# Kernel optimization log

Hardware: AMD Instinct MI355X
Metric: run time of the kernel (lower is better)

The kernel has to match this reference:

```python
import jax, jax.numpy as jnp
import numpy as np

B_CHUNK = 5          # hardcoded self.B in the module
GAMMA = 0.9865
BATCH, SEQ, FEAT, DIM = 8, 4000, 256, 256


def setup_inputs() -> dict:
    key = jax.random.key(0)
    ks = jax.random.split(key, 6)
    xq = jax.random.normal(ks[0], (BATCH, SEQ, FEAT), jnp.float32)
    xk = jax.random.normal(ks[1], (BATCH, SEQ, FEAT), jnp.float32)
    xv = jax.random.normal(ks[2], (BATCH, SEQ, FEAT), jnp.float32)
    scale = 1.0 / np.sqrt(FEAT).astype(np.float32)
    Wq = jax.random.normal(ks[3], (FEAT, DIM), jnp.float32) * scale
    Wk = jax.random.normal(ks[4], (FEAT, DIM), jnp.float32) * scale
    Wv = jax.random.normal(ks[5], (FEAT, DIM), jnp.float32) * scale
    return {"xq": xq, "xk": xk, "xv": xv, "Wq": Wq, "Wk": Wk, "Wv": Wv}


def reference(xq, xk, xv, Wq, Wk, Wv):
    gamma = jnp.float32(GAMMA)
    B = B_CHUNK
    b, seq, _ = xq.shape
    dim = Wq.shape[1]
    n = seq // B  # number of chunks

    # projections, chunked: [b, n, B, dim]
    Q = (xq @ Wq).reshape(b, n, B, dim)
    K = (xk @ Wk).reshape(b, n, B, dim)
    V = (xv @ Wv).reshape(b, n, B, dim)

    chunk_idx = jnp.arange(n, dtype=jnp.float32)
    # Z[i] = gamma^(B - i - 1) (per-chunk scalar, as in original)
    Z = gamma ** (jnp.float32(B) - chunk_idx - 1.0)
    Vz = V * Z[None, :, None, None]

    # intra-chunk decay matrix: L[i,j] = gamma^(j-i) for i >= j, else 0
    pos = jnp.arange(B, dtype=jnp.float32)
    L = jnp.tril(gamma ** (pos[None, :] - pos[:, None]))

    # intra-chunk term: (Q K^T * L) @ V, vectorized over all chunks
    S = jnp.einsum('bnid,bnjd->bnij', Q, K)          # [b, n, B, B]
    intra = jnp.einsum('bnij,bnjd->bnid', S * L, V)  # [b, n, B, dim]

    # cross-chunk recurrence: R[i] = K_i^T Vz_i + gamma^B R[i-1]
    # X[i-1] += Q_i @ R[i-1] * gamma^(i+1)
    Qn = jnp.moveaxis(Q, 1, 0)   # [n, b, B, dim]
    Kn = jnp.moveaxis(K, 1, 0)
    Vzn = jnp.moveaxis(Vz, 1, 0)
    gB = gamma ** B

    def step(R_prev, inp):
        qi, ki, vzi, i = inp
        cross_prev = jnp.einsum('bod,bde->boe', qi, R_prev) * gamma ** (i + 1.0)
        R_new = jnp.einsum('bod,boe->bde', ki, vzi) + gB * R_prev
        return R_new, cross_prev

    R0 = jnp.zeros((b, dim, dim), xq.dtype)
    _, ys = jax.lax.scan(step, R0, (Qn, Kn, Vzn, chunk_idx))  # ys[i] = cross for chunk i-1
    cross = jnp.concatenate([ys[1:], jnp.zeros_like(ys[:1])], axis=0)  # last chunk has no cross term
    cross = jnp.moveaxis(cross, 0, 1)  # [b, n, B, dim]

    X = intra + cross
    return X.reshape(b, seq, dim)
```

## Files before the change

### kernel.cpp

```cpp
#include <hip/hip_runtime.h>
#include <cmath>

#define GAMMA 0.9865f
#define L2G   -0.01960905f
#define BATCH 8
#define SEQ   4000
#define CSUP  25
#define GSUP  32
#define RPG   125

typedef _Float16 half8 __attribute__((ext_vector_type(8)));
typedef _Float16 half4 __attribute__((ext_vector_type(4)));
typedef float    floatx4 __attribute__((ext_vector_type(4)));

__device__ __forceinline__ float gpow(float e) { return exp2f(e * L2G); }

__global__ __launch_bounds__(256) void wt_convert(
    const float* __restrict__ Wq, const float* __restrict__ Wk, const float* __restrict__ Wv,
    _Float16* __restrict__ Wt) {
    int t = blockIdx.x * 256 + threadIdx.x;
    int mat = t >> 16, rem = t & 65535;
    int n = rem >> 8, k = rem & 255;
    const float* W = (mat == 0) ? Wq : (mat == 1) ? Wk : Wv;
    Wt[(size_t)mat * 65536 + n * 256 + k] = (_Float16)W[k * 256 + n];
}

__global__ __launch_bounds__(256, 2) void qkv_gemm_f16(
    const float* __restrict__ xq, const float* __restrict__ xk, const float* __restrict__ xv,
    const _Float16* __restrict__ WtAll,
    _Float16* __restrict__ Qb, _Float16* __restrict__ Kb, _Float16* __restrict__ Vb) {
    int op = blockIdx.y;
    const float* x = (op == 0) ? xq : (op == 1) ? xk : xv;
    const _Float16* Wt = WtAll + (size_t)op * 65536;
    _Float16* dst = (op == 0) ? Qb : (op == 1) ? Kb : Vb;

    __shared__ _Float16 Xs[2][128][40];
    __shared__ _Float16 WsT[2][256][40];

    int t = threadIdx.x;
    int lane = t & 63, wave = t >> 6;
    int ln = lane & 15, q8 = (lane >> 4) << 3, q4 = (lane >> 4) << 2;
    int row0 = blockIdx.x * 128;

    int xm = t >> 3, xk_ = (t & 7) << 2;
    int wr = t >> 2, wk = (t & 3) << 3;

    floatx4 acc[8][4] = {};
    floatx4 xn[4]; half8 wn[4];

    auto loadNext = [&](int dt) {
        int k0 = dt * 32;
#pragma unroll
        for (int i = 0; i < 4; ++i)
            xn[i] = *(const floatx4*)&x[(size_t)(row0 + xm + i * 32) * 256 + k0 + xk_];
#pragma unroll
        for (int i = 0; i < 4; ++i)
            wn[i] = *(const half8*)&Wt[(wr + i * 64) * 256 + k0 + wk];
    };
    auto writeBuf = [&](int bf) {
#pragma unroll
        for (int i = 0; i < 4; ++i) {
            half4 h; h[0] = (_Float16)xn[i][0]; h[1] = (_Float16)xn[i][1];
            h[2] = (_Float16)xn[i][2]; h[3] = (_Float16)xn[i][3];
            *(half4*)&Xs[bf][xm + i * 32][xk_] = h;
        }
#pragma unroll
        for (int i = 0; i < 4; ++i)
            *(half8*)&WsT[bf][wr + i * 64][wk] = wn[i];
    };

    loadNext(0); writeBuf(0);
    int cur = 0;
    for (int dt = 0; dt < 8; ++dt) {
        __syncthreads();
        if (dt < 7) loadNext(dt + 1);
        half8 af[8];
#pragma unroll
        for (int mi = 0; mi < 8; ++mi) af[mi] = *(const half8*)&Xs[cur][mi * 16 + ln][q8];
#pragma unroll
        for (int ni = 0; ni < 4; ++ni) {
            half8 bf = *(const half8*)&WsT[cur][(wave * 4 + ni) * 16 + ln][q8];
#pragma unroll
            for (int mi = 0; mi < 8; ++mi)
                acc[mi][ni] = __builtin_amdgcn_mfma_f32_16x16x32_f16(af[mi], bf, acc[mi][ni], 0, 0, 0);
        }
        if (dt < 7) { writeBuf(cur ^ 1); cur ^= 1; }
    }
#pragma unroll
    for (int mi = 0; mi < 8; ++mi)
#pragma unroll
        for (int ni = 0; ni < 4; ++ni)
#pragma unroll
            for (int r = 0; r < 4; ++r) {
                int row = row0 + mi * 16 + q4 + r;
                int col = (wave * 4 + ni) * 16 + ln;
                dst[(size_t)row * 256 + col] = (_Float16)acc[mi][ni][r];
            }
}

__global__ __launch_bounds__(256) void vt_transpose(
    const _Float16* __restrict__ Vb, _Float16* __restrict__ VT) {
    int es = blockIdx.x, g = blockIdx.y, b = blockIdx.z;
    int t = threadIdx.x;
    __shared__ __align__(16) _Float16 Ls[64 * 136];
#pragma unroll
    for (int i = 0; i < 4; ++i) {
        int idx = t + i * 256;
        int cp = idx >> 3, eg = idx & 7;
        half8 v = {};
        if (cp < 125)
            v = *(const half8*)&Vb[((size_t)b * SEQ + g * RPG + cp) * 256 + es * 64 + eg * 8];
        int cpg = cp >> 3, c7 = cp & 7;
#pragma unroll
        for (int z = 0; z < 8; ++z) {
            int e = eg * 8 + z;
            Ls[e * 136 + ((cpg ^ (e >> 3)) << 3) + c7] = v[z];
        }
    }
    __syncthreads();
#pragma unroll
    for (int jj = 0; jj < 4; ++jj) {
        int ee = jj * 16 + (t >> 4);
        int cpg = t & 15;
        half8 h = *(const half8*)&Ls[ee * 136 + ((cpg ^ (ee >> 3)) << 3)];
        *(half8*)&VT[(((size_t)b * 256 + es * 64 + ee) * 32 + g) * 128 + cpg * 8] = h;
    }
}

__global__ __launch_bounds__(256, 2) void chunk_states_mfma(
    const _Float16* __restrict__ Kb, const _Float16* __restrict__ Vb,
    _Float16* __restrict__ Wh) {
    int eh = blockIdx.x, g = blockIdx.y, b = blockIdx.z;
    int t = threadIdx.x, lane = t & 63, wave = t >> 6;
    int ln = lane & 15, q8 = (lane >> 4) << 3, q4 = (lane >> 4) << 2;
    __shared__ __align__(16) _Float16 Vs[32 * 136];
    __shared__ __align__(16) _Float16 Ks[32 * 264];
    size_t base_row = (size_t)b * SEQ + g * RPG;
    floatx4 acc[8][4] = {};
    for (int kt = 0; kt < 4; ++kt) {
        int r0 = kt * 32;
#pragma unroll
        for (int i = 0; i < 2; ++i) {
            int idx = t + i * 256;
            int r = idx >> 4, e8 = (idx & 15) << 3;
            half8 v = {};
            if (r0 + r < RPG) {
                v = *(const half8*)&Vb[(base_row + r0 + r) * 256 + eh * 128 + e8];
                int mloc = (r0 + r) / 5;
                float a = gpow((float)(149 - 6 * mloc));
#pragma unroll
                for (int z = 0; z < 8; ++z) v[z] = (_Float16)((float)v[z] * a);
            }
            *(half8*)&Vs[r * 136 + e8] = v;
        }
#pragma unroll
        for (int i = 0; i < 4; ++i) {
            int idx = t + i * 256;
            int r = idx >> 5, d8 = (idx & 31) << 3;
            half8 v = {};
            if (r0 + r < RPG) v = *(const half8*)&Kb[(base_row + r0 + r) * 256 + d8];
            *(half8*)&Ks[r * 264 + d8] = v;
        }
        __syncthreads();
        half8 Af[8], Bf[4];
#pragma unroll
        for (int mi = 0; mi < 8; ++mi)
#pragma unroll
            for (int j = 0; j < 8; ++j) Af[mi][j] = Vs[(q8 + j) * 136 + mi * 16 + ln];
#pragma unroll
        for (int ni = 0; ni < 4; ++ni)
#pragma unroll
            for (int j = 0; j < 8; ++j) Bf[ni][j] = Ks[(q8 + j) * 264 + wave * 64 + ni * 16 + ln];
#pragma unroll
        for (int mi = 0; mi < 8; ++mi)
#pragma unroll
            for (int ni = 0; ni < 4; ++ni)
                acc[mi][ni] = __builtin_amdgcn_mfma_f32_16x16x32_f16(Af[mi], Bf[ni], acc[mi][ni], 0, 0, 0);
        __syncthreads();
    }
    size_t ob = ((size_t)(g * 8 + b)) << 16;
#pragma unroll
    for (int mi = 0; mi < 8; ++mi)
#pragma unroll
        for (int ni = 0; ni < 4; ++ni)
#pragma unroll
            for (int r = 0; r < 4; ++r) {
                int e = eh * 128 + mi * 16 + q4 + r;
                int d = wave * 64 + ni * 16 + ln;
                Wh[ob + (size_t)e * 256 + d] = (_Float16)acc[mi][ni][r];
            }
}

__global__ __launch_bounds__(256) void state_scan(
    const _Float16* __restrict__ Wh, _Float16* __restrict__ SprevT) {
    int t = blockIdx.x * 256 + threadIdx.x;
    int b = t >> 14;
    int idx = (t & 16383) << 2;
    const float gF = gpow(150.0f);
    float s[4] = {};
    half4 w = *(const half4*)&Wh[(((size_t)b) << 16) + idx];
    for (int g = 0; g < GSUP; ++g) {
        size_t o = (((size_t)(g * 8 + b)) << 16) + idx;
        half4 wn = {};
        if (g < GSUP - 1) wn = *(const half4*)&Wh[o + (8ull << 16)];
        half4 sv;
#pragma unroll
        for (int z = 0; z < 4; ++z) { sv[z] = (_Float16)s[z]; s[z] = (float)w[z] + gF * s[z]; }
        *(half4*)&SprevT[o] = sv;
        w = wn;
    }
}

__global__ __launch_bounds__(256) void intra_sc(
    const _Float16* __restrict__ Qb, const _Float16* __restrict__ Kb, float* __restrict__ scw) {
    int b = blockIdx.y;
    int j = blockIdx.x * 4 + (threadIdx.x >> 6);
    int lane = threadIdx.x & 63;
    size_t base = ((size_t)b * SEQ + j * 5) * 256 + lane * 4;
    half4 qv[5], kv[5];
#pragma unroll
    for (int p = 0; p < 5; ++p) {
        qv[p] = *(const half4*)&Qb[base + p * 256];
        kv[p] = *(const half4*)&Kb[base + p * 256];
    }
#pragma unroll
    for (int p = 0; p < 5; ++p)
#pragma unroll
        for (int q = 0; q <= p; ++q) {
            float s = 0.f;
#pragma unroll
            for (int z = 0; z < 4; ++z) s += (float)qv[p][z] * (float)kv[q][z];
#pragma unroll
            for (int off = 32; off; off >>= 1) s += __shfl_xor(s, off, 64);
            if (lane == 0) scw[((size_t)b * 800 + j) * 25 + p * 5 + q] = s * gpow((float)(q - p));
        }
}

__global__ __launch_bounds__(512, 2) void cross_f16(
    const _Float16* __restrict__ Qb, const _Float16* __restrict__ Kb,
    const _Float16* __restrict__ VT, const _Float16* __restrict__ SprevT,
    const float* __restrict__ scw, float* __restrict__ out) {
    int eq = blockIdx.x, g = blockIdx.y, b = blockIdx.z;
    int e0 = eq * 64;
    int t = threadIdx.x;
    int lane = t & 63, wave = t >> 6;
    int ln = lane & 15, q8 = (lane >> 4) << 3, q4 = (lane >> 4) << 2;
    int mw = wave;

    __shared__ __align__(16) char smem[52224];
    _Float16* QsB  = (_Float16*)smem;
    _Float16* KsB  = (_Float16*)(smem + 20480);
    _Float16* SsB  = (_Float16*)(smem + 40960);
    _Float16* VsTB = (_Float16*)smem;
    _Float16* PsB  = (_Float16*)(smem + 17408);
#define QS(bf_, m_, k_)  QsB[(bf_) * 5120 + (m_) * 40 + (k_)]
#define KS(bf_, m_, k_)  KsB[(bf_) * 5120 + (m_) * 40 + (k_)]
#define SS(bf_, m_, k_)  SsB[(bf_) * 2560 + (m_) * 40 + (k_)]
#define PS(m_, k_)  PsB[(m_) * 136 + (k_)]
#define VST(m_, k_) VsTB[(m_) * 136 + (k_)]

    size_t kvbase = (size_t)b * SEQ + g * RPG;
    size_t sb = ((size_t)(g * 8 + b)) << 16;

    int qm = t >> 2, qk = (t & 3) << 3;
    int vm = t >> 3, vc = t & 7;

    floatx4 pacc[8] = {};
    floatx4 acc[4] = {};
    half8 qn, kn, sn;
    half8 vtp[2];

    auto loadNext = [&](int dt) {
        int d0 = dt * 32;
        half8 z = {};
        int qr = g * RPG + 5 + qm;
        qn = z;
        if (qm < 125 && qr < SEQ) qn = *(const half8*)&Qb[((size_t)b * SEQ + qr) * 256 + d0 + qk];
        kn = z;
        if (qm < 125) kn = *(const half8*)&Kb[(kvbase + qm) * 256 + d0 + qk];
        if (t < 256) sn = *(const half8*)&SprevT[sb + (size_t)(e0 + (t >> 2)) * 256 + d0 + qk];
    };
    auto writeBuf = [&](int bf) {
        *(half8*)&QS(bf, qm, qk) = qn;
        *(half8*)&KS(bf, qm, qk) = kn;
        if (t < 256) *(half8*)&SS(bf, t >> 2, qk) = sn;
    };

    loadNext(0); writeBuf(0);
    int cur = 0;
    for (int dt = 0; dt < 8; ++dt) {
        __syncthreads();
        if (dt < 7) loadNext(dt + 1);
        if (dt == 7) {
            size_t vtbase = (((size_t)b * 256 + e0 + vm) * 32 + g) * 128;
            vtp[0] = *(const half8*)&VT[vtbase + vc * 8];
            vtp[1] = *(const half8*)&VT[vtbase + (vc + 8) * 8];
        }
        half8 af = *(const half8*)&QS(cur, mw * 16 + ln, q8);
#pragma unroll
        for (int ci = 0; ci < 8; ++ci) {
            half8 bf = *(const half8*)&KS(cur, ci * 16 + ln, q8);
            pacc[ci] = __builtin_amdgcn_mfma_f32_16x16x32_f16(af, bf, pacc[ci], 0, 0, 0);
        }
#pragma unroll
        for (int ei = 0; ei < 4; ++ei) {
            half8 sf = *(const half8*)&SS(cur, ei * 16 + ln, q8);
            acc[ei] = __builtin_amdgcn_mfma_f32_16x16x32_f16(af, sf, acc[ei], 0, 0, 0);
        }
        if (dt < 7) { writeBuf(cur ^ 1); cur ^= 1; }
    }

#pragma unroll
    for (int r = 0; r < 4; ++r) {
        int rp = mw * 16 + q4 + r;
        int rc = rp / 5;
        float rs = 0.f;
        if (rp < 125 && !(g == GSUP - 1 && rc == CSUP - 1)) rs = gpow((float)(6 * rc + 7));
#pragma unroll
        for (int ei = 0; ei < 4; ++ei) acc[ei][r] *= rs;
    }

    __syncthreads();

    *(half8*)&VST(vm, vc << 3) = vtp[0];
    *(half8*)&VST(vm, (vc + 8) << 3) = vtp[1];
#pragma unroll
    for (int ci = 0; ci < 8; ++ci)
#pragma unroll
        for (int r = 0; r < 4; ++r) {
            int rp = mw * 16 + q4 + r;
            int cp = ci * 16 + ln;
            int rc = rp / 5, cc = cp / 5;
            float w = 0.f;
            if (rp < 125 && cp < 125 && cc <= rc && !(g == GSUP - 1 && rc == CSUP - 1))
                w = gpow((float)(6 * (rc - cc + 1)));
            PS(rp, cp) = (_Float16)(pacc[ci][r] * w);
        }
    __syncthreads();

#pragma unroll
    for (int ct = 0; ct < 4; ++ct) {
        int cp0 = ct * 32;
        half8 paf = *(const half8*)&PS(mw * 16 + ln, cp0 + q8);
#pragma unroll
        for (int ei = 0; ei < 4; ++ei) {
            half8 bv = *(const half8*)&VST(ei * 16 + ln, cp0 + q8);
            acc[ei] = __builtin_amdgcn_mfma_f32_16x16x32_f16(paf, bv, acc[ei], 0, 0, 0);
        }
    }

#pragma unroll
    for (int r = 0; r < 4; ++r) {
        int rp = mw * 16 + q4 + r;
        if (rp < 125) {
            int rc = rp / 5, pp = rp - rc * 5;
            const float* srow = scw + ((size_t)b * 800 + g * 25 + rc) * 25 + pp * 5;
            float a[4];
#pragma unroll
            for (int ei = 0; ei < 4; ++ei) a[ei] = acc[ei][r];
            for (int q = 0; q <= pp; ++q) {
                float s = srow[q];
#pragma unroll
                for (int ei = 0; ei < 4; ++ei)
                    a[ei] += s * (float)VST(ei * 16 + ln, rc * 5 + q);
            }
            size_t orow = ((size_t)b * SEQ + g * RPG + rp) * 256;
#pragma unroll
            for (int ei = 0; ei < 4; ++ei)
                out[orow + e0 + ei * 16 + ln] = a[ei];
        }
    }
}

extern "C" void kernel_launch(void* const* d_in, const int* in_sizes, int n_in,
                              void* d_out, int out_size, void* d_ws, size_t ws_size,
                              hipStream_t stream) {
    const float* xq = (const float*)d_in[0];
    const float* xk = (const float*)d_in[1];
    const float* xv = (const float*)d_in[2];
    const float* Wq = (const float*)d_in[3];
    const float* Wk = (const float*)d_in[4];
    const float* Wv = (const float*)d_in[5];
    float* out = (float*)d_out;

    const size_t NELEM = (size_t)SEQ * BATCH * 256;
    _Float16* Qb = (_Float16*)d_ws;
    _Float16* Kb = Qb + NELEM;
    _Float16* Vb = Kb + NELEM;
    _Float16* Wt = Vb + NELEM;
    _Float16* Wh = Wt + 196608;
    _Float16* SprevT = Wh + (size_t)GSUP * BATCH * 65536;
    float* scw = (float*)(SprevT + (size_t)GSUP * BATCH * 65536);
    _Float16* VT = Wh;

    wt_convert<<<dim3(768), 256, 0, stream>>>(Wq, Wk, Wv, Wt);
    qkv_gemm_f16<<<dim3(250, 3), 256, 0, stream>>>(xq, xk, xv, Wt, Qb, Kb, Vb);
    chunk_states_mfma<<<dim3(2, 32, 8), 256, 0, stream>>>(Kb, Vb, Wh);
    state_scan<<<dim3(512), 256, 0, stream>>>(Wh, SprevT);
    vt_transpose<<<dim3(4, 32, 8), 256, 0, stream>>>(Vb, VT);
    intra_sc<<<dim3(200, 8), 256, 0, stream>>>(Qb, Kb, scw);
    cross_f16<<<dim3(4, 32, 8), 512, 0, stream>>>(Qb, Kb, VT, SprevT, scw, out);
}
```

Measured before the change: 253.7 us.

## Transpose and swizzle LDS tiles in chunk_states; XCD-aware block remapping

In chunk_states_mfma, V and K tiles are now stored transposed in LDS with an XOR swizzle, so each MFMA operand fragment is one 16-byte vector load instead of eight scalar strided reads. This cuts LDS read instructions and bank conflicts, but the stores become eight scalar writes per thread. Both chunk_states_mfma and cross_f16 also remap the linear block id so consecutive blocks spread across the 8 XCDs, aiming for better L2 locality.

```diff
diff --git a/kernel.cpp b/kernel.cpp
--- a/kernel.cpp
+++ b/kernel.cpp
@@ -130,13 +130,17 @@
 __global__ __launch_bounds__(256, 2) void chunk_states_mfma(
     const _Float16* __restrict__ Kb, const _Float16* __restrict__ Vb,
     _Float16* __restrict__ Wh) {
-    int eh = blockIdx.x, g = blockIdx.y, b = blockIdx.z;
+    int lin = blockIdx.x + 2 * (blockIdx.y + 32 * blockIdx.z);
+    int swz = (lin & 7) * 64 + (lin >> 3);
+    int eh = swz & 1, g = (swz >> 1) & 31, b = swz >> 6;
+
     int t = threadIdx.x, lane = t & 63, wave = t >> 6;
     int ln = lane & 15, q8 = (lane >> 4) << 3, q4 = (lane >> 4) << 2;
-    __shared__ __align__(16) _Float16 Vs[32 * 136];
-    __shared__ __align__(16) _Float16 Ks[32 * 264];
+    __shared__ __align__(16) _Float16 VsT[128 * 40];
+    __shared__ __align__(16) _Float16 KsT[256 * 40];
     size_t base_row = (size_t)b * SEQ + g * RPG;
     floatx4 acc[8][4] = {};
+    int rb = q8 >> 3;
     for (int kt = 0; kt < 4; ++kt) {
         int r0 = kt * 32;
 #pragma unroll
@@ -151,7 +155,9 @@
 #pragma unroll
                 for (int z = 0; z < 8; ++z) v[z] = (_Float16)((float)v[z] * a);
             }
-            *(half8*)&Vs[r * 136 + e8] = v;
+            int base = e8 * 40 + ((((r >> 3) ^ ((e8 >> 3) & 3))) << 3) + (r & 7);
+#pragma unroll
+            for (int z = 0; z < 8; ++z) VsT[base + z * 40] = v[z];
         }
 #pragma unroll
         for (int i = 0; i < 4; ++i) {
@@ -159,18 +165,22 @@
             int r = idx >> 5, d8 = (idx & 31) << 3;
             half8 v = {};
             if (r0 + r < RPG) v = *(const half8*)&Kb[(base_row + r0 + r) * 256 + d8];
-            *(half8*)&Ks[r * 264 + d8] = v;
+            int base = d8 * 40 + ((((r >> 3) ^ ((d8 >> 3) & 3))) << 3) + (r & 7);
+#pragma unroll
+            for (int z = 0; z < 8; ++z) KsT[base + z * 40] = v[z];
         }
         __syncthreads();
         half8 Af[8], Bf[4];
 #pragma unroll
-        for (int mi = 0; mi < 8; ++mi)
-#pragma unroll
-            for (int j = 0; j < 8; ++j) Af[mi][j] = Vs[(q8 + j) * 136 + mi * 16 + ln];
-#pragma unroll
-        for (int ni = 0; ni < 4; ++ni)
-#pragma unroll
-            for (int j = 0; j < 8; ++j) Bf[ni][j] = Ks[(q8 + j) * 264 + wave * 64 + ni * 16 + ln];
+        for (int mi = 0; mi < 8; ++mi) {
+            int e = mi * 16 + ln;
+            Af[mi] = *(const half8*)&VsT[e * 40 + ((rb ^ ((e >> 3) & 3)) << 3)];
+        }
+#pragma unroll
+        for (int ni = 0; ni < 4; ++ni) {
+            int d = wave * 64 + ni * 16 + ln;
+            Bf[ni] = *(const half8*)&KsT[d * 40 + ((rb ^ ((d >> 3) & 3)) << 3)];
+        }
 #pragma unroll
         for (int mi = 0; mi < 8; ++mi)
 #pragma unroll
@@ -240,7 +250,9 @@
     const _Float16* __restrict__ Qb, const _Float16* __restrict__ Kb,
     const _Float16* __restrict__ VT, const _Float16* __restrict__ SprevT,
     const float* __restrict__ scw, float* __restrict__ out) {
-    int eq = blockIdx.x, g = blockIdx.y, b = blockIdx.z;
+    int lin = blockIdx.x + 4 * (blockIdx.y + 32 * blockIdx.z);
+    int swz = (lin & 7) * 128 + (lin >> 3);
+    int eq = swz & 3, g = (swz >> 2) & 31, b = swz >> 7;
     int e0 = eq * 64;
     int t = threadIdx.x;
     int lane = t & 63, wave = t >> 6;
```

Result: faster. 244.4 us, median of 2 (-3.7%).
